# Performance work log

Hardware: AMD Instinct MI355X
Metric: run time of the kernel (lower is better)

Reference implementation:

```python
import jax, jax.numpy as jnp
import numpy as np

L, H, A, NREL2 = 3, 64, 64, 474
N_NODE, N_EDGE, B = 100000, 1000000, 32


def setup_inputs() -> dict:
    key = jax.random.key(0)
    ks = jax.random.split(key, 20)
    f = jax.random.normal
    s = 0.05
    return dict(
        sub_idx=jax.random.randint(ks[0], (N_EDGE,), 0, N_NODE),
        rel_idx=jax.random.randint(ks[1], (N_EDGE,), 0, NREL2),
        obj_idx=jax.random.randint(ks[2], (N_EDGE,), 0, N_NODE),
        edge_batch=jax.random.randint(ks[3], (N_EDGE,), 0, B),
        q_rel=jax.random.randint(ks[4], (B,), 0, NREL2),
        query_sub_idxs=jax.random.randint(ks[5], (B,), 0, N_NODE),
        rela_embed=f(ks[6], (L, NREL2, H)) * s,
        query_rela_embed=f(ks[7], (NREL2, H)) * s,
        Ws=f(ks[8], (L, H, A)) * s,
        Wr=f(ks[9], (L, H, A)) * s,
        Wqr=f(ks[10], (L, H, A)) * s,
        bqr=f(ks[11], (L, A)) * s,
        w_alpha=f(ks[12], (L, A)) * s,
        b_alpha=f(ks[13], (L,)) * s,
        W_h=f(ks[14], (L, H, H)) * s,
        gru_Wih=f(ks[15], (L, 3 * H, H)) * s,
        gru_Whh=f(ks[16], (L, 3 * H, H)) * s,
        gru_bih=f(ks[17], (L, 3 * H)) * s,
        gru_bhh=f(ks[18], (L, 3 * H)) * s,
        W_final=f(ks[19], (H,)) * s,
        n_node=N_NODE,
    )


def reference(sub_idx, rel_idx, obj_idx, edge_batch, q_rel, query_sub_idxs,
              rela_embed, query_rela_embed, Ws, Wr, Wqr, bqr, w_alpha, b_alpha,
              W_h, gru_Wih, gru_Whh, gru_bih, gru_bhh, W_final, n_node):
    # initializer='relation': seed query-subject nodes with query relation embedding
    hidden = jnp.zeros((n_node, H), jnp.float32).at[query_sub_idxs].set(query_rela_embed[q_rel])
    h0 = jnp.zeros((n_node, H), jnp.float32)  # GRU state

    for l in range(L):
        # ---- GNNLayer: gather -> attention MLP -> scatter-add ----
        hs = hidden[sub_idx]                       # [E, H]
        hr = rela_embed[l][rel_idx]                # [E, H]
        h_qr = rela_embed[l][q_rel][edge_batch]    # [E, H] query-rel emb per edge
        pre = jax.nn.relu(hs @ Ws[l] + hr @ Wr[l] + h_qr @ Wqr[l] + bqr[l])  # [E, A]
        alpha = jax.nn.sigmoid(pre @ w_alpha[l] + b_alpha[l])[:, None]       # [E, 1]
        msg = alpha * (hs * hr)                                              # [E, H]
        agg = jax.ops.segment_sum(msg, obj_idx, num_segments=n_node)        # [N, H]
        hidden = jax.nn.relu(agg @ W_h[l])

        # act_signal: mask untouched nodes (detached in original)
        mask = jnp.where(jax.lax.stop_gradient(jnp.sum(hidden, -1)) == 0, 0.0, 1.0)[:, None]

        # ---- one GRU step per node (PyTorch GRU math) ----
        gi = hidden @ gru_Wih[l].T + gru_bih[l]   # [N, 3H]
        gh = h0 @ gru_Whh[l].T + gru_bhh[l]       # [N, 3H]
        i_r, i_z, i_n = jnp.split(gi, 3, axis=-1)
        h_r, h_z, h_n = jnp.split(gh, 3, axis=-1)
        r = jax.nn.sigmoid(i_r + h_r)
        z = jax.nn.sigmoid(i_z + h_z)
        n = jnp.tanh(i_n + r * h_n)
        h_new = (1.0 - z) * n + z * h0
        hidden = h_new * mask
        h0 = h_new * mask

    # readout='linear', no bias
    scores = hidden @ W_final                     # [N]
    return scores
```

## Files before the change

### kernel.cpp

```cpp
#include <hip/hip_runtime.h>
#include <hip/hip_bf16.h>

#define NL 3
#define HD 64
#define TCAP 1024
#define NB 8

typedef unsigned char u8;

__device__ __forceinline__ float sigf(float x){ return 1.f/(1.f+__expf(-x)); }

__device__ __forceinline__ float wsum(float v){
  #pragma unroll
  for (int off=32; off; off>>=1) v += __shfl_xor(v, off, 64);
  return v;
}

__device__ __forceinline__ float bcastf(float v, int l){
  return __int_as_float(__builtin_amdgcn_readlane(__float_as_int(v), l));
}

__device__ __forceinline__ float ldin(const void* p, size_t i, int bf){
  return bf ? __bfloat162float(((const __hip_bfloat16*)p)[i]) : ((const float*)p)[i];
}

__device__ __forceinline__ bool testbit(const unsigned* __restrict__ w, int n){
  return (w[n>>5] >> (n&31)) & 1u;
}

__device__ __forceinline__ int probe_bf(const void* probe, int lane){
  unsigned short h = ((const unsigned short*)probe)[lane];
  int e = (h >> 7) & 0xFF;
  int sane = ((h & 0x7FFF) == 0) || (e >= 96 && e <= 132);
  unsigned long long m = __ballot(sane != 0);
  return (__popcll(m) >= 56) ? 1 : 0;
}

__global__ void __launch_bounds__(256) k_setup(
    const void* __restrict__ W_h, const void* __restrict__ Ws,
    const void* __restrict__ Wih, const void* __restrict__ Whh,
    const void* __restrict__ bih, const void* __restrict__ bhh,
    const void* __restrict__ wal, const void* __restrict__ bal,
    const void* __restrict__ Wf,  const void* __restrict__ rel,
    const void* __restrict__ Wr,  const void* __restrict__ Wqr,
    const void* __restrict__ bqr, const void* __restrict__ qre,
    const int* __restrict__ q_rel, const int* __restrict__ qsub,
    float* __restrict__ WhF, float* __restrict__ WsF,
    float* __restrict__ WiT, float* __restrict__ WhT,
    float* __restrict__ biF, float* __restrict__ bhF,
    float* __restrict__ waF, float* __restrict__ baF,
    float* __restrict__ WfF, float* __restrict__ REL,
    float* __restrict__ R2, float* __restrict__ QR,
    float* __restrict__ hid, float* __restrict__ HS2, unsigned* __restrict__ liveW,
    int* __restrict__ stamp, int* __restrict__ plist, int* __restrict__ pcnt,
    int NR, int B, int PB, int TB)
{
  int lane = threadIdx.x & 63;
  int bf = probe_bf(rel, lane);

  if ((int)blockIdx.x < PB){
    int j = blockIdx.x*256 + threadIdx.x;
    const int sWT = NL*HD*HD, sWI = NL*192*HD, sB = NL*192;
    if (j < sWT){ WhF[j]=ldin(W_h,j,bf); return; } j-=sWT;
    if (j < sWT){ WsF[j]=ldin(Ws ,j,bf); return; } j-=sWT;
    if (j < sWI){ int l=j/(192*HD), q=j%(192*HD), h=q/192, a=q%192;
                  WiT[j]=ldin(Wih,(size_t)l*192*HD + (size_t)a*HD + h,bf); return; } j-=sWI;
    if (j < sWI){ int l=j/(192*HD), q=j%(192*HD), h=q/192, a=q%192;
                  WhT[j]=ldin(Whh,(size_t)l*192*HD + (size_t)a*HD + h,bf); return; } j-=sWI;
    if (j < sB){ biF[j]=ldin(bih,j,bf); return; } j-=sB;
    if (j < sB){ bhF[j]=ldin(bhh,j,bf); return; } j-=sB;
    if (j < NL*HD){ waF[j]=ldin(wal,j,bf); return; } j-=NL*HD;
    if (j < NL){ baF[j]=ldin(bal,j,bf); return; } j-=NL;
    if (j < HD){ WfF[j]=ldin(Wf,j,bf); return; } j-=HD;
    if (j < NL*NR*HD){ REL[j]=ldin(rel,j,bf); return; }
    return;
  }
  if ((int)blockIdx.x < PB+TB){
    int bid = ((int)blockIdx.x - PB)*4 + (threadIdx.x>>6);
    if (bid < NL*NR){
      int l = bid/NR, r = bid%NR;
      float x = ldin(rel,(size_t)(l*NR+r)*HD + lane,bf);
      float acc = 0.f;
      #pragma unroll
      for (int h=0; h<HD; ++h)
        acc = fmaf(bcastf(x, h), ldin(Wr,(size_t)(l*HD+h)*HD + lane,bf), acc);
      R2[(size_t)bid*HD + lane] = acc;
    } else if (bid < NL*NR + NL*B){
      int b2 = bid - NL*NR;
      int l = b2/B, b = b2%B;
      int r = q_rel[b];
      float x = ldin(rel,(size_t)(l*NR+r)*HD + lane,bf);
      float acc = ldin(bqr,(size_t)l*HD + lane,bf);
      #pragma unroll
      for (int h=0; h<HD; ++h)
        acc = fmaf(bcastf(x, h), ldin(Wqr,(size_t)(l*HD+h)*HD + lane,bf), acc);
      QR[(size_t)b2*HD + lane] = acc;
    }
    return;
  }
  int b = ((int)blockIdx.x - PB - TB)*4 + (threadIdx.x>>6);
  if (b >= B) return;
  int n = qsub[b];
  for (int b2 = b+1; b2 < B; ++b2) if (qsub[b2] == n) return;
  int r = q_rel[b];
  float v = ldin(qre,(size_t)r*HD + lane,bf);
  hid[(size_t)n*HD + lane] = v;
  float acc = 0.f;
  #pragma unroll 8
  for (int h=0; h<HD; ++h)
    acc = fmaf(bcastf(v,h), ldin(Ws,(size_t)h*HD + lane,bf), acc);
  HS2[(size_t)n*HD + lane] = acc;
  if (lane==0){
    atomicOr(&liveW[n>>5], 1u<<(n&31));
    stamp[n] = 1;
    int idx = atomicAdd(pcnt, 1);
    plist[idx] = n;
  }
}

__global__ void __launch_bounds__(256) k_edge(
    const int* __restrict__ sub, const int* __restrict__ rel_i,
    const int* __restrict__ obj, const int* __restrict__ eb,
    const unsigned* __restrict__ liveW,
    const float* __restrict__ hid, const float* __restrict__ HS2,
    const float* __restrict__ R2l, const float* __restrict__ QRl,
    const float* __restrict__ RELl, const float* __restrict__ waFl,
    const float* __restrict__ baFl, float* __restrict__ agg,
    int* __restrict__ stamp, int* __restrict__ tlist, int* __restrict__ tcnt,
    int ep, int E)
{
  __shared__ int s_cnt;
  __shared__ int s_base;
  __shared__ int s_buf[TCAP];
  if (threadIdx.x == 0) s_cnt = 0;
  __syncthreads();

  int lane = threadIdx.x & 63;
  int wid = (blockIdx.x*256 + threadIdx.x) >> 6;
  int nw = gridDim.x*4;
  long long stride = (long long)nw*256;
  float wa = waFl[lane];
  float ba = baFl[0];

  long long base0 = (long long)wid*256;
  int4 s4 = make_int4(0,0,0,0);
  if (base0 + 256 <= E)
    s4 = *reinterpret_cast<const int4*>(&sub[base0 + 4*(long long)lane]);

  for (long long base = base0; base < E; base += stride){
    bool vec = (base + 256 <= E);
    long long nbase = base + stride;
    int4 s4n = make_int4(0,0,0,0);
    bool nvec = (nbase < E) && (nbase + 256 <= E);
    if (nvec)
      s4n = *reinterpret_cast<const int4*>(&sub[nbase + 4*(long long)lane]);

    unsigned long long m[4];
    if (vec){
      m[0] = __ballot(testbit(liveW, s4.x));
      m[1] = __ballot(testbit(liveW, s4.y));
      m[2] = __ballot(testbit(liveW, s4.z));
      m[3] = __ballot(testbit(liveW, s4.w));
    } else {
      #pragma unroll
      for (int j=0;j<4;++j){
        long long e = base + 4*(long long)lane + j;
        bool lv = (e < E) && testbit(liveW, sub[e]);
        m[j] = __ballot(lv);
      }
    }
    #pragma unroll
    for (int j=0;j<4;++j){
      unsigned long long mask = m[j];
      while (mask){
        int bit = (int)__ffsll(mask) - 1;
        mask &= mask - 1;
        long long ee = base + 4*(long long)bit + j;
        int ss = sub[ee], r = rel_i[ee], o = obj[ee], b = eb[ee];
        float hs  = hid[(size_t)ss*HD + lane];
        float pre = HS2[(size_t)ss*HD + lane] + R2l[(size_t)r*HD + lane] + QRl[(size_t)b*HD + lane];
        pre = fmaxf(pre, 0.f);
        float alpha = sigf(wsum(pre*wa) + ba);
        unsafeAtomicAdd(&agg[(size_t)o*HD + lane], alpha * hs * RELl[(size_t)r*HD + lane]);
        if (lane==0){
          int old = atomicExch(&stamp[o], ep);
          if (old != ep){
            int li = atomicAdd(&s_cnt, 1);
            if (li < TCAP) s_buf[li] = o;
            else { int gi = atomicAdd(tcnt, 1); tlist[gi] = o; }
          }
        }
      }
    }
    s4 = s4n;
  }

  __syncthreads();
  int cnt = s_cnt; if (cnt > TCAP) cnt = TCAP;
  if (threadIdx.x == 0 && cnt > 0) s_base = atomicAdd(tcnt, cnt);
  __syncthreads();
  if (cnt > 0){
    int b0 = s_base;
    for (int i = threadIdx.x; i < cnt; i += 256) tlist[b0 + i] = s_buf[i];
  }
}

__global__ void __launch_bounds__(256) k_node(
    const int* __restrict__ tlist, const int* __restrict__ tcnt,
    float* __restrict__ agg, float* __restrict__ hid, float* __restrict__ HS2,
    unsigned* __restrict__ liveW,
    const float* __restrict__ WhFl,
    const float* __restrict__ WiTl,
    const float* __restrict__ WhTl,
    const float* __restrict__ biFl, const float* __restrict__ bhFl,
    const float* __restrict__ WsFn,
    const float* __restrict__ WfF,
    const int* __restrict__ plist, const int* __restrict__ pcnt,
    const int* __restrict__ stamp,
    float* __restrict__ out, int N, int isFirst, int isLast, int ep)
{
  int cntv = tcnt[0]; if (cntv > N) cntv = N;
  int lane = threadIdx.x & 63;
  int wid = (blockIdx.x*256 + threadIdx.x) >> 6;
  int nw = gridDim.x*4;
  float bi0=biFl[lane], bi1=biFl[HD+lane], bi2=biFl[2*HD+lane];
  float bh0=bhFl[lane], bh1=bhFl[HD+lane], bh2=bhFl[2*HD+lane];
  float wfv = isLast ? WfF[lane] : 0.f;

  for (int i0 = wid*NB; i0 < cntv; i0 += nw*NB){
    int nd[NB]; bool val[NB]; bool wp[NB]; float av[NB];
    #pragma unroll
    for (int j=0;j<NB;++j){
      val[j] = (i0+j) < cntv;
      nd[j]  = tlist[val[j] ? (i0+j) : i0];
      wp[j]  = (!isFirst) && val[j] && testbit(liveW, nd[j]);
      av[j]  = val[j] ? agg[(size_t)nd[j]*HD + lane] : 0.f;
    }
    if (!isLast){
      #pragma unroll
      for (int j=0;j<NB;++j) if (val[j]) agg[(size_t)nd[j]*HD + lane] = 0.f;
    }

    float hm[NB];
    #pragma unroll
    for (int j=0;j<NB;++j) hm[j] = 0.f;
    #pragma unroll 8
    for (int h=0; h<HD; ++h){
      float w = WhFl[h*HD + lane];
      #pragma unroll
      for (int j=0;j<NB;++j) hm[j] = fmaf(bcastf(av[j],h), w, hm[j]);
    }
    float mask[NB]; float h0v[NB];
    #pragma unroll
    for (int j=0;j<NB;++j){
      hm[j] = fmaxf(hm[j], 0.f);
      mask[j] = (__ballot(hm[j] != 0.f) != 0ull) ? 1.f : 0.f;
      h0v[j] = wp[j] ? hid[(size_t)nd[j]*HD + lane] : 0.f;
    }

    float gi0[NB], gi1[NB], gi2[NB], gh0[NB], gh1[NB], gh2[NB];
    #pragma unroll
    for (int j=0;j<NB;++j){ gi0[j]=bi0; gi1[j]=bi1; gi2[j]=bi2; gh0[j]=bh0; gh1[j]=bh1; gh2[j]=bh2; }
    #pragma unroll 4
    for (int h=0; h<HD; ++h){
      const float* __restrict__ wr = WiTl + (size_t)h*192;
      float w0 = wr[lane], w1 = wr[64+lane], w2 = wr[128+lane];
      #pragma unroll
      for (int j=0;j<NB;++j){
        float x = bcastf(hm[j],h);
        gi0[j] = fmaf(x, w0, gi0[j]);
        gi1[j] = fmaf(x, w1, gi1[j]);
        gi2[j] = fmaf(x, w2, gi2[j]);
      }
    }
    #pragma unroll
    for (int j=0;j<NB;++j){
      if (wp[j]){
        #pragma unroll 4
        for (int h=0; h<HD; ++h){
          const float* __restrict__ wr = WhTl + (size_t)h*192;
          float y = bcastf(h0v[j],h);
          gh0[j] = fmaf(y, wr[lane],     gh0[j]);
          gh1[j] = fmaf(y, wr[64+lane],  gh1[j]);
          gh2[j] = fmaf(y, wr[128+lane], gh2[j]);
        }
      }
    }

    float hn[NB];
    #pragma unroll
    for (int j=0;j<NB;++j){
      float r = sigf(gi0[j]+gh0[j]);
      float z = sigf(gi1[j]+gh1[j]);
      float nn = tanhf(gi2[j] + r*gh2[j]);
      hn[j] = ((1.f - z)*nn + z*h0v[j])*mask[j];
    }

    if (isLast){
      #pragma unroll
      for (int j=0;j<NB;++j){
        float sc = wsum(hn[j] * wfv);
        if (lane==0 && val[j]) out[nd[j]] = sc;
      }
      continue;
    }
    #pragma unroll
    for (int j=0;j<NB;++j){
      unsigned long long lv = __ballot(hn[j] != 0.f);
      if (val[j]){
        hid[(size_t)nd[j]*HD + lane] = hn[j];
        if (lane==0){
          unsigned bit = 1u << (nd[j]&31);
          if (lv) atomicOr (&liveW[nd[j]>>5],  bit);
          else    atomicAnd(&liveW[nd[j]>>5], ~bit);
        }
      }
    }

    float acc[NB];
    #pragma unroll
    for (int j=0;j<NB;++j) acc[j] = 0.f;
    #pragma unroll 8
    for (int h=0; h<HD; ++h){
      float w = WsFn[h*HD + lane];
      #pragma unroll
      for (int j=0;j<NB;++j) acc[j] = fmaf(bcastf(hn[j],h), w, acc[j]);
    }
    #pragma unroll
    for (int j=0;j<NB;++j) if (val[j]) HS2[(size_t)nd[j]*HD + lane] = acc[j];
  }

  if (!isLast){
    int pc = pcnt[0]; if (pc > N) pc = N;
    for (int i = blockIdx.x*256 + threadIdx.x; i < pc; i += gridDim.x*256){
      int n = plist[i];
      if (stamp[n] != ep) atomicAnd(&liveW[n>>5], ~(1u<<(n&31)));
    }
  }
}

extern "C" void kernel_launch(void* const* d_in, const int* in_sizes, int n_in,
                              void* d_out, int out_size, void* d_ws, size_t ws_size,
                              hipStream_t stream)
{
  const int* sub   = (const int*)d_in[0];
  const int* rel_i = (const int*)d_in[1];
  const int* obj   = (const int*)d_in[2];
  const int* eb    = (const int*)d_in[3];
  const int* q_rel = (const int*)d_in[4];
  const int* qsub  = (const int*)d_in[5];
  const void* rela = d_in[6];
  const void* qre  = d_in[7];
  const void* Wsp  = d_in[8];
  const void* Wr   = d_in[9];
  const void* Wqr  = d_in[10];
  const void* bqr  = d_in[11];
  const void* wal  = d_in[12];
  const void* bal  = d_in[13];
  const void* W_h  = d_in[14];
  const void* Wih  = d_in[15];
  const void* Whh  = d_in[16];
  const void* bih  = d_in[17];
  const void* bhh  = d_in[18];
  const void* Wf   = d_in[19];

  int E  = in_sizes[0];
  int B  = in_sizes[4];
  int NR = in_sizes[6]/(NL*HD);
  int N  = out_size;
  int NW = (N + 31) / 32;

  float* ws = (float*)d_ws;
  size_t o = 0;
  float* agg  = ws + o; o += (size_t)N*HD;
  int*   stamp= (int*)(ws + o); o += N;
  int*   cnts = (int*)(ws + o); o += 16;
  unsigned* liveW = (unsigned*)(ws + o); o += NW;
  float* hid  = ws + o; o += (size_t)N*HD;
  float* HS2  = ws + o; o += (size_t)N*HD;
  float* R2   = ws + o; o += (size_t)NL*NR*HD;
  float* QR   = ws + o; o += (size_t)NL*B*HD;
  float* REL  = ws + o; o += (size_t)NL*NR*HD;
  float* WhF  = ws + o; o += NL*HD*HD;
  float* WsF  = ws + o; o += NL*HD*HD;
  float* WiT  = ws + o; o += NL*192*HD;
  float* WhT  = ws + o; o += NL*192*HD;
  float* biF  = ws + o; o += NL*192;
  float* bhF  = ws + o; o += NL*192;
  float* waF  = ws + o; o += NL*HD;
  float* baF  = ws + o; o += NL;
  float* WfF  = ws + o; o += HD;
  int*   listA= (int*)(ws + o); o += N;
  int*   listB= (int*)(ws + o); o += N;

  size_t z1 = (size_t)N*HD*sizeof(float) + (size_t)N*sizeof(int)
            + 16*sizeof(int) + (size_t)NW*sizeof(unsigned);
  hipMemsetAsync(agg, 0, z1, stream);
  hipMemsetAsync(d_out, 0, (size_t)N*sizeof(float), stream);

  int prepN = 2*(NL*HD*HD) + 2*(NL*192*HD) + 2*(NL*192) + NL*HD + NL + HD + NL*NR*HD;
  int PB = (prepN + 255)/256;
  int TB = (NL*NR + NL*B + 3)/4;
  int IB = (B + 3)/4;
  k_setup<<<PB + TB + IB, 256, 0, stream>>>(
      W_h, Wsp, Wih, Whh, bih, bhh, wal, bal, Wf, rela, Wr, Wqr, bqr, qre,
      q_rel, qsub,
      WhF, WsF, WiT, WhT, biF, bhF, waF, baF, WfF, REL, R2, QR,
      hid, HS2, liveW, stamp, listA, cnts+3, NR, B, PB, TB);

  int* curT = listB;
  int* prevL = listA;
  for (int l=0; l<NL; ++l){
    int ep = l + 2;
    k_edge<<<2048, 256, 0, stream>>>(sub, rel_i, obj, eb, liveW, hid, HS2,
        R2 + (size_t)l*NR*HD, QR + (size_t)l*B*HD, REL + (size_t)l*NR*HD,
        waF + l*HD, baF + l, agg, stamp, curT, cnts+4+l, ep, E);
    k_node<<<2048, 256, 0, stream>>>(curT, cnts+4+l, agg, hid, HS2, liveW,
        WhF + (size_t)l*HD*HD, WiT + (size_t)l*192*HD, WhT + (size_t)l*192*HD,
        biF + l*192, bhF + l*192,
        (l < NL-1) ? (WsF + (size_t)(l+1)*HD*HD) : WsF,
        WfF,
        prevL, (l==0) ? (cnts+3) : (cnts+4+l-1), stamp,
        (float*)d_out, N, (l==0)?1:0, (l==NL-1)?1:0, ep);
    int* t = prevL; prevL = curT; curT = t;
  }
}
```

Measured before the change: 172.5 us.

## Fuse per-layer edge and node kernels into one persistent cooperative kernel

Replaces the six separate edge/node kernel launches with a single cooperative persistent kernel that loops over layers and uses grid-wide syncs between the edge scatter phase and the node GRU phase. The goal is to remove launch overhead and inter-kernel gaps for a workload where each layer touches few active nodes. The grid shrinks from 2048 blocks to at most 960, capped by occupancy, which reduces parallelism in the edge scan and adds grid-sync cost.

```diff
diff --git a/kernel.cpp b/kernel.cpp
--- a/kernel.cpp
+++ b/kernel.cpp
@@ -1,5 +1,8 @@
 #include <hip/hip_runtime.h>
 #include <hip/hip_bf16.h>
+#include <hip/hip_cooperative_groups.h>
+
+namespace cg = cooperative_groups;
 
 #define NL 3
 #define HD 64
@@ -118,224 +121,238 @@
   }
 }
 
-__global__ void __launch_bounds__(256) k_edge(
-    const int* __restrict__ sub, const int* __restrict__ rel_i,
-    const int* __restrict__ obj, const int* __restrict__ eb,
-    const unsigned* __restrict__ liveW,
-    const float* __restrict__ hid, const float* __restrict__ HS2,
-    const float* __restrict__ R2l, const float* __restrict__ QRl,
-    const float* __restrict__ RELl, const float* __restrict__ waFl,
-    const float* __restrict__ baFl, float* __restrict__ agg,
-    int* __restrict__ stamp, int* __restrict__ tlist, int* __restrict__ tcnt,
-    int ep, int E)
+struct KP {
+  const int *sub, *rel_i, *obj, *eb;
+  float *agg, *hid, *HS2;
+  unsigned *liveW;
+  int *stamp, *cnts, *listA, *listB;
+  const float *R2, *QR, *REL;
+  const float *WhF, *WsF, *WiT, *WhT, *biF, *bhF, *waF, *baF, *WfF;
+  float *out;
+  int E, N, NR, B;
+};
+
+__global__ void __launch_bounds__(256, 4) k_main(KP p)
 {
+  cg::grid_group grid = cg::this_grid();
   __shared__ int s_cnt;
   __shared__ int s_base;
   __shared__ int s_buf[TCAP];
-  if (threadIdx.x == 0) s_cnt = 0;
-  __syncthreads();
 
   int lane = threadIdx.x & 63;
   int wid = (blockIdx.x*256 + threadIdx.x) >> 6;
   int nw = gridDim.x*4;
-  long long stride = (long long)nw*256;
-  float wa = waFl[lane];
-  float ba = baFl[0];
-
-  long long base0 = (long long)wid*256;
-  int4 s4 = make_int4(0,0,0,0);
-  if (base0 + 256 <= E)
-    s4 = *reinterpret_cast<const int4*>(&sub[base0 + 4*(long long)lane]);
-
-  for (long long base = base0; base < E; base += stride){
-    bool vec = (base + 256 <= E);
-    long long nbase = base + stride;
-    int4 s4n = make_int4(0,0,0,0);
-    bool nvec = (nbase < E) && (nbase + 256 <= E);
-    if (nvec)
-      s4n = *reinterpret_cast<const int4*>(&sub[nbase + 4*(long long)lane]);
-
-    unsigned long long m[4];
-    if (vec){
-      m[0] = __ballot(testbit(liveW, s4.x));
-      m[1] = __ballot(testbit(liveW, s4.y));
-      m[2] = __ballot(testbit(liveW, s4.z));
-      m[3] = __ballot(testbit(liveW, s4.w));
-    } else {
-      #pragma unroll
-      for (int j=0;j<4;++j){
-        long long e = base + 4*(long long)lane + j;
-        bool lv = (e < E) && testbit(liveW, sub[e]);
-        m[j] = __ballot(lv);
+
+  int* prevL = p.listA;
+  const int* prevCnt = p.cnts + 3;
+  int* curT = p.listB;
+
+  for (int l = 0; l < NL; ++l){
+    int ep = l + 2;
+    const float* __restrict__ R2l  = p.R2  + (size_t)l*p.NR*HD;
+    const float* __restrict__ QRl  = p.QR  + (size_t)l*p.B*HD;
+    const float* __restrict__ RELl = p.REL + (size_t)l*p.NR*HD;
+    int* tcnt = p.cnts + 4 + l;
+
+    if (threadIdx.x == 0) s_cnt = 0;
+    __syncthreads();
+    {
+      float wa = p.waF[l*HD + lane];
+      float ba = p.baF[l];
+      long long stride = (long long)nw*256;
+      long long base0 = (long long)wid*256;
+      int4 s4 = make_int4(0,0,0,0);
+      if (base0 + 256 <= p.E)
+        s4 = *reinterpret_cast<const int4*>(&p.sub[base0 + 4*(long long)lane]);
+
+      for (long long base = base0; base < p.E; base += stride){
+        bool vec = (base + 256 <= p.E);
+        long long nbase = base + stride;
+        int4 s4n = make_int4(0,0,0,0);
+        if (nbase < p.E && nbase + 256 <= p.E)
+          s4n = *reinterpret_cast<const int4*>(&p.sub[nbase + 4*(long long)lane]);
+
+        unsigned long long m[4];
+        if (vec){
+          m[0] = __ballot(testbit(p.liveW, s4.x));
+          m[1] = __ballot(testbit(p.liveW, s4.y));
+          m[2] = __ballot(testbit(p.liveW, s4.z));
+          m[3] = __ballot(testbit(p.liveW, s4.w));
+        } else {
+          #pragma unroll
+          for (int j=0;j<4;++j){
+            long long e = base + 4*(long long)lane + j;
+            bool lv = (e < p.E) && testbit(p.liveW, p.sub[e]);
+            m[j] = __ballot(lv);
+          }
+        }
+        #pragma unroll
+        for (int j=0;j<4;++j){
+          unsigned long long mask = m[j];
+          while (mask){
+            int bit = (int)__ffsll(mask) - 1;
+            mask &= mask - 1;
+            long long ee = base + 4*(long long)bit + j;
+            int ss = p.sub[ee], r = p.rel_i[ee], o = p.obj[ee], b = p.eb[ee];
+            float hs  = p.hid[(size_t)ss*HD + lane];
+            float pre = p.HS2[(size_t)ss*HD + lane] + R2l[(size_t)r*HD + lane] + QRl[(size_t)b*HD + lane];
+            pre = fmaxf(pre, 0.f);
+            float alpha = sigf(wsum(pre*wa) + ba);
+            unsafeAtomicAdd(&p.agg[(size_t)o*HD + lane], alpha * hs * RELl[(size_t)r*HD + lane]);
+            if (lane==0){
+              int old = atomicExch(&p.stamp[o], ep);
+              if (old != ep){
+                int li = atomicAdd(&s_cnt, 1);
+                if (li < TCAP) s_buf[li] = o;
+                else { int gi = atomicAdd(tcnt, 1); curT[gi] = o; }
+              }
+            }
+          }
+        }
+        s4 = s4n;
       }
     }
-    #pragma unroll
-    for (int j=0;j<4;++j){
-      unsigned long long mask = m[j];
-      while (mask){
-        int bit = (int)__ffsll(mask) - 1;
-        mask &= mask - 1;
-        long long ee = base + 4*(long long)bit + j;
-        int ss = sub[ee], r = rel_i[ee], o = obj[ee], b = eb[ee];
-        float hs  = hid[(size_t)ss*HD + lane];
-        float pre = HS2[(size_t)ss*HD + lane] + R2l[(size_t)r*HD + lane] + QRl[(size_t)b*HD + lane];
-        pre = fmaxf(pre, 0.f);
-        float alpha = sigf(wsum(pre*wa) + ba);
-        unsafeAtomicAdd(&agg[(size_t)o*HD + lane], alpha * hs * RELl[(size_t)r*HD + lane]);
-        if (lane==0){
-          int old = atomicExch(&stamp[o], ep);
-          if (old != ep){
-            int li = atomicAdd(&s_cnt, 1);
-            if (li < TCAP) s_buf[li] = o;
-            else { int gi = atomicAdd(tcnt, 1); tlist[gi] = o; }
-          }
-        }
+    __syncthreads();
+    {
+      int cnt = s_cnt; if (cnt > TCAP) cnt = TCAP;
+      if (threadIdx.x == 0 && cnt > 0) s_base = atomicAdd(tcnt, cnt);
+      __syncthreads();
+      if (cnt > 0){
+        int b0 = s_base;
+        for (int i = threadIdx.x; i < cnt; i += 256) curT[b0 + i] = s_buf[i];
       }
     }
-    s4 = s4n;
-  }
-
-  __syncthreads();
-  int cnt = s_cnt; if (cnt > TCAP) cnt = TCAP;
-  if (threadIdx.x == 0 && cnt > 0) s_base = atomicAdd(tcnt, cnt);
-  __syncthreads();
-  if (cnt > 0){
-    int b0 = s_base;
-    for (int i = threadIdx.x; i < cnt; i += 256) tlist[b0 + i] = s_buf[i];
-  }
-}
-
-__global__ void __launch_bounds__(256) k_node(
-    const int* __restrict__ tlist, const int* __restrict__ tcnt,
-    float* __restrict__ agg, float* __restrict__ hid, float* __restrict__ HS2,
-    unsigned* __restrict__ liveW,
-    const float* __restrict__ WhFl,
-    const float* __restrict__ WiTl,
-    const float* __restrict__ WhTl,
-    const float* __restrict__ biFl, const float* __restrict__ bhFl,
-    const float* __restrict__ WsFn,
-    const float* __restrict__ WfF,
-    const int* __restrict__ plist, const int* __restrict__ pcnt,
-    const int* __restrict__ stamp,
-    float* __restrict__ out, int N, int isFirst, int isLast, int ep)
-{
-  int cntv = tcnt[0]; if (cntv > N) cntv = N;
-  int lane = threadIdx.x & 63;
-  int wid = (blockIdx.x*256 + threadIdx.x) >> 6;
-  int nw = gridDim.x*4;
-  float bi0=biFl[lane], bi1=biFl[HD+lane], bi2=biFl[2*HD+lane];
-  float bh0=bhFl[lane], bh1=bhFl[HD+lane], bh2=bhFl[2*HD+lane];
-  float wfv = isLast ? WfF[lane] : 0.f;
-
-  for (int i0 = wid*NB; i0 < cntv; i0 += nw*NB){
-    int nd[NB]; bool val[NB]; bool wp[NB]; float av[NB];
-    #pragma unroll
-    for (int j=0;j<NB;++j){
-      val[j] = (i0+j) < cntv;
-      nd[j]  = tlist[val[j] ? (i0+j) : i0];
-      wp[j]  = (!isFirst) && val[j] && testbit(liveW, nd[j]);
-      av[j]  = val[j] ? agg[(size_t)nd[j]*HD + lane] : 0.f;
-    }
-    if (!isLast){
-      #pragma unroll
-      for (int j=0;j<NB;++j) if (val[j]) agg[(size_t)nd[j]*HD + lane] = 0.f;
-    }
-
-    float hm[NB];
-    #pragma unroll
-    for (int j=0;j<NB;++j) hm[j] = 0.f;
-    #pragma unroll 8
-    for (int h=0; h<HD; ++h){
-      float w = WhFl[h*HD + lane];
-      #pragma unroll
-      for (int j=0;j<NB;++j) hm[j] = fmaf(bcastf(av[j],h), w, hm[j]);
-    }
-    float mask[NB]; float h0v[NB];
-    #pragma unroll
-    for (int j=0;j<NB;++j){
-      hm[j] = fmaxf(hm[j], 0.f);
-      mask[j] = (__ballot(hm[j] != 0.f) != 0ull) ? 1.f : 0.f;
-      h0v[j] = wp[j] ? hid[(size_t)nd[j]*HD + lane] : 0.f;
-    }
-
-    float gi0[NB], gi1[NB], gi2[NB], gh0[NB], gh1[NB], gh2[NB];
-    #pragma unroll
-    for (int j=0;j<NB;++j){ gi0[j]=bi0; gi1[j]=bi1; gi2[j]=bi2; gh0[j]=bh0; gh1[j]=bh1; gh2[j]=bh2; }
-    #pragma unroll 4
-    for (int h=0; h<HD; ++h){
-      const float* __restrict__ wr = WiTl + (size_t)h*192;
-      float w0 = wr[lane], w1 = wr[64+lane], w2 = wr[128+lane];
-      #pragma unroll
-      for (int j=0;j<NB;++j){
-        float x = bcastf(hm[j],h);
-        gi0[j] = fmaf(x, w0, gi0[j]);
-        gi1[j] = fmaf(x, w1, gi1[j]);
-        gi2[j] = fmaf(x, w2, gi2[j]);
+    grid.sync();
+
+    {
+      int cntv = tcnt[0]; if (cntv > p.N) cntv = p.N;
+      int isFirst = (l==0), isLast = (l==NL-1);
+      const float* __restrict__ WhFl = p.WhF + (size_t)l*HD*HD;
+      const float* __restrict__ WiTl = p.WiT + (size_t)l*192*HD;
+      const float* __restrict__ WhTl = p.WhT + (size_t)l*192*HD;
+      const float* __restrict__ biFl = p.biF + l*192;
+      const float* __restrict__ bhFl = p.bhF + l*192;
+      const float* __restrict__ WsFn = (l < NL-1) ? (p.WsF + (size_t)(l+1)*HD*HD) : p.WsF;
+      float bi0=biFl[lane], bi1=biFl[HD+lane], bi2=biFl[2*HD+lane];
+      float bh0=bhFl[lane], bh1=bhFl[HD+lane], bh2=bhFl[2*HD+lane];
+      float wfv = isLast ? p.WfF[lane] : 0.f;
+
+      for (int i0 = wid*NB; i0 < cntv; i0 += nw*NB){
+        int nd[NB]; bool val[NB]; bool wp[NB]; float av[NB];
+        #pragma unroll
+        for (int j=0;j<NB;++j){
+          val[j] = (i0+j) < cntv;
+          nd[j]  = curT[val[j] ? (i0+j) : i0];
+          wp[j]  = (!isFirst) && val[j] && testbit(p.liveW, nd[j]);
+          av[j]  = val[j] ? p.agg[(size_t)nd[j]*HD + lane] : 0.f;
+        }
+        if (!isLast){
+          #pragma unroll
+          for (int j=0;j<NB;++j) if (val[j]) p.agg[(size_t)nd[j]*HD + lane] = 0.f;
+        }
+
+        float hm[NB];
+        #pragma unroll
+        for (int j=0;j<NB;++j) hm[j] = 0.f;
+        #pragma unroll 8
+        for (int h=0; h<HD; ++h){
+          float w = WhFl[h*HD + lane];
+          #pragma unroll
+          for (int j=0;j<NB;++j) hm[j] = fmaf(bcastf(av[j],h), w, hm[j]);
+        }
+        float mask[NB]; float h0v[NB];
+        #pragma unroll
+        for (int j=0;j<NB;++j){
+          hm[j] = fmaxf(hm[j], 0.f);
+          mask[j] = (__ballot(hm[j] != 0.f) != 0ull) ? 1.f : 0.f;
+          h0v[j] = wp[j] ? p.hid[(size_t)nd[j]*HD + lane] : 0.f;
+        }
+
+        float gi0[NB], gi1[NB], gi2[NB], gh0[NB], gh1[NB], gh2[NB];
+        #pragma unroll
+        for (int j=0;j<NB;++j){ gi0[j]=bi0; gi1[j]=bi1; gi2[j]=bi2; gh0[j]=bh0; gh1[j]=bh1; gh2[j]=bh2; }
+        #pragma unroll 4
+        for (int h=0; h<HD; ++h){
+          const float* __restrict__ wr = WiTl + (size_t)h*192;
+          float w0 = wr[lane], w1 = wr[64+lane], w2 = wr[128+lane];
+          #pragma unroll
+          for (int j=0;j<NB;++j){
+            float x = bcastf(hm[j],h);
+            gi0[j] = fmaf(x, w0, gi0[j]);
+            gi1[j] = fmaf(x, w1, gi1[j]);
+            gi2[j] = fmaf(x, w2, gi2[j]);
+          }
+        }
+        #pragma unroll
+        for (int j=0;j<NB;++j){
+          if (wp[j]){
+            #pragma unroll 4
+            for (int h=0; h<HD; ++h){
+              const float* __restrict__ wr = WhTl + (size_t)h*192;
+              float y = bcastf(h0v[j],h);
+              gh0[j] = fmaf(y, wr[lane],     gh0[j]);
+              gh1[j] = fmaf(y, wr[64+lane],  gh1[j]);
+              gh2[j] = fmaf(y, wr[128+lane], gh2[j]);
+            }
+          }
+        }
+
+        float hn[NB];
+        #pragma unroll
+        for (int j=0;j<NB;++j){
+          float r = sigf(gi0[j]+gh0[j]);
+          float z = sigf(gi1[j]+gh1[j]);
+          float nn = tanhf(gi2[j] + r*gh2[j]);
+          hn[j] = ((1.f - z)*nn + z*h0v[j])*mask[j];
+        }
+
+        if (isLast){
+          #pragma unroll
+          for (int j=0;j<NB;++j){
+            float sc = wsum(hn[j] * wfv);
+            if (lane==0 && val[j]) p.out[nd[j]] = sc;
+          }
+          continue;
+        }
+        #pragma unroll
+        for (int j=0;j<NB;++j){
+          unsigned long long lv = __ballot(hn[j] != 0.f);
+          if (val[j]){
+            p.hid[(size_t)nd[j]*HD + lane] = hn[j];
+            if (lane==0){
+              unsigned bit = 1u << (nd[j]&31);
+              if (lv) atomicOr (&p.liveW[nd[j]>>5],  bit);
+              else    atomicAnd(&p.liveW[nd[j]>>5], ~bit);
+            }
+          }
+        }
+
+        float acc[NB];
+        #pragma unroll
+        for (int j=0;j<NB;++j) acc[j] = 0.f;
+        #pragma unroll 8
+        for (int h=0; h<HD; ++h){
+          float w = WsFn[h*HD + lane];
+          #pragma unroll
+          for (int j=0;j<NB;++j) acc[j] = fmaf(bcastf(hn[j],h), w, acc[j]);
+        }
+        #pragma unroll
+        for (int j=0;j<NB;++j) if (val[j]) p.HS2[(size_t)nd[j]*HD + lane] = acc[j];
+      }
+
+      if (!isLast){
+        int pc = prevCnt[0]; if (pc > p.N) pc = p.N;
+        for (int i = blockIdx.x*256 + threadIdx.x; i < pc; i += gridDim.x*256){
+          int n = prevL[i];
+          if (p.stamp[n] != ep) atomicAnd(&p.liveW[n>>5], ~(1u<<(n&31)));
+        }
       }
     }
-    #pragma unroll
-    for (int j=0;j<NB;++j){
-      if (wp[j]){
-        #pragma unroll 4
-        for (int h=0; h<HD; ++h){
-          const float* __restrict__ wr = WhTl + (size_t)h*192;
-          float y = bcastf(h0v[j],h);
-          gh0[j] = fmaf(y, wr[lane],     gh0[j]);
-          gh1[j] = fmaf(y, wr[64+lane],  gh1[j]);
-          gh2[j] = fmaf(y, wr[128+lane], gh2[j]);
-        }
-      }
-    }
-
-    float hn[NB];
-    #pragma unroll
-    for (int j=0;j<NB;++j){
-      float r = sigf(gi0[j]+gh0[j]);
-      float z = sigf(gi1[j]+gh1[j]);
-      float nn = tanhf(gi2[j] + r*gh2[j]);
-      hn[j] = ((1.f - z)*nn + z*h0v[j])*mask[j];
-    }
-
-    if (isLast){
-      #pragma unroll
-      for (int j=0;j<NB;++j){
-        float sc = wsum(hn[j] * wfv);
-        if (lane==0 && val[j]) out[nd[j]] = sc;
-      }
-      continue;
-    }
-    #pragma unroll
-    for (int j=0;j<NB;++j){
-      unsigned long long lv = __ballot(hn[j] != 0.f);
-      if (val[j]){
-        hid[(size_t)nd[j]*HD + lane] = hn[j];
-        if (lane==0){
-          unsigned bit = 1u << (nd[j]&31);
-          if (lv) atomicOr (&liveW[nd[j]>>5],  bit);
-          else    atomicAnd(&liveW[nd[j]>>5], ~bit);
-        }
-      }
-    }
-
-    float acc[NB];
-    #pragma unroll
-    for (int j=0;j<NB;++j) acc[j] = 0.f;
-    #pragma unroll 8
-    for (int h=0; h<HD; ++h){
-      float w = WsFn[h*HD + lane];
-      #pragma unroll
-      for (int j=0;j<NB;++j) acc[j] = fmaf(bcastf(hn[j],h), w, acc[j]);
-    }
-    #pragma unroll
-    for (int j=0;j<NB;++j) if (val[j]) HS2[(size_t)nd[j]*HD + lane] = acc[j];
-  }
-
-  if (!isLast){
-    int pc = pcnt[0]; if (pc > N) pc = N;
-    for (int i = blockIdx.x*256 + threadIdx.x; i < pc; i += gridDim.x*256){
-      int n = plist[i];
-      if (stamp[n] != ep) atomicAnd(&liveW[n>>5], ~(1u<<(n&31)));
-    }
+    grid.sync();
+
+    prevL = curT;
+    prevCnt = tcnt;
+    curT = (curT == p.listB) ? p.listA : p.listB;
   }
 }
 
@@ -408,20 +425,24 @@
       WhF, WsF, WiT, WhT, biF, bhF, waF, baF, WfF, REL, R2, QR,
       hid, HS2, liveW, stamp, listA, cnts+3, NR, B, PB, TB);
 
-  int* curT = listB;
-  int* prevL = listA;
-  for (int l=0; l<NL; ++l){
-    int ep = l + 2;
-    k_edge<<<2048, 256, 0, stream>>>(sub, rel_i, obj, eb, liveW, hid, HS2,
-        R2 + (size_t)l*NR*HD, QR + (size_t)l*B*HD, REL + (size_t)l*NR*HD,
-        waF + l*HD, baF + l, agg, stamp, curT, cnts+4+l, ep, E);
-    k_node<<<2048, 256, 0, stream>>>(curT, cnts+4+l, agg, hid, HS2, liveW,
-        WhF + (size_t)l*HD*HD, WiT + (size_t)l*192*HD, WhT + (size_t)l*192*HD,
-        biF + l*192, bhF + l*192,
-        (l < NL-1) ? (WsF + (size_t)(l+1)*HD*HD) : WsF,
-        WfF,
-        prevL, (l==0) ? (cnts+3) : (cnts+4+l-1), stamp,
-        (float*)d_out, N, (l==0)?1:0, (l==NL-1)?1:0, ep);
-    int* t = prevL; prevL = curT; curT = t;
+  KP kp;
+  kp.sub = sub; kp.rel_i = rel_i; kp.obj = obj; kp.eb = eb;
+  kp.agg = agg; kp.hid = hid; kp.HS2 = HS2;
+  kp.liveW = liveW; kp.stamp = stamp; kp.cnts = cnts;
+  kp.listA = listA; kp.listB = listB;
+  kp.R2 = R2; kp.QR = QR; kp.REL = REL;
+  kp.WhF = WhF; kp.WsF = WsF; kp.WiT = WiT; kp.WhT = WhT;
+  kp.biF = biF; kp.bhF = bhF; kp.waF = waF; kp.baF = baF; kp.WfF = WfF;
+  kp.out = (float*)d_out;
+  kp.E = E; kp.N = N; kp.NR = NR; kp.B = B;
+
+  int grid = 960;
+  int maxb = 0;
+  if (hipOccupancyMaxActiveBlocksPerMultiprocessor(&maxb, k_main, 256, 0) == hipSuccess
+      && maxb > 0){
+    int cap = maxb * 256;
+    if (grid > cap) grid = cap;
   }
-}
+  void* args[] = { &kp };
+  hipLaunchCooperativeKernel((const void*)k_main, dim3(grid), dim3(256), args, 0, stream);
+}
```

After: 642.3 us. 272% more time.
